# Performance work log

Hardware: AMD Instinct MI355X
Metric: run time of the kernel (lower is better)

## Reference

```python
import math
import jax, jax.numpy as jnp
import numpy as np

DEPTH, HEADS, DIM, MLP = 12, 16, 1024, 4096
J, P0, B = 17, 256, 8
N0 = J + P0
HD = DIM // HEADS
SCALE = DIM ** -0.5  # scale_with_head=False -> dim**-0.5
PRUNE_LOC = (3, 6, 9)
KEEP = 0.7


def setup_inputs() -> dict:
    key = jax.random.key(0)
    ks = jax.random.split(key, 8)
    rn = lambda k, shape, s=0.02: jax.random.normal(k, shape, dtype=jnp.float32) * s
    # rotary table (cos, sin) per position, replicated per layer: [DEPTH, N0, HD/2, 2]
    inv = 1.0 / (10000.0 ** (np.arange(0, HD, 2, dtype=np.float64) / HD))
    ang = np.arange(N0, dtype=np.float64)[:, None] * inv[None, :]
    fc = np.stack([np.cos(ang), np.sin(ang)], axis=-1)[None]
    freqs_cis = jnp.asarray(np.broadcast_to(fc, (DEPTH, N0, HD // 2, 2)), jnp.float32)
    return dict(
        x=jax.random.normal(ks[0], (B, N0, DIM), jnp.float32),
        freqs_cis=freqs_cis,
        learnable_absolute=jnp.ones((DEPTH,), jnp.float32),
        pos=rn(ks[1], (1, P0, DIM)),
        ln1_g=jnp.ones((DEPTH, DIM), jnp.float32), ln1_b=jnp.zeros((DEPTH, DIM), jnp.float32),
        w_qkv=rn(ks[2], (DEPTH, 3 * DIM, DIM)),
        w_out=rn(ks[3], (DEPTH, DIM, DIM)), b_out=jnp.zeros((DEPTH, DIM), jnp.float32),
        ln2_g=jnp.ones((DEPTH, DIM), jnp.float32), ln2_b=jnp.zeros((DEPTH, DIM), jnp.float32),
        w1=rn(ks[4], (DEPTH, MLP, DIM)), b1=jnp.zeros((DEPTH, MLP), jnp.float32),
        w2=rn(ks[5], (DEPTH, DIM, MLP)), b2=jnp.zeros((DEPTH, DIM), jnp.float32),
    )


def _ln(x, g, b, eps=1e-5):
    m = x.mean(-1, keepdims=True)
    v = ((x - m) ** 2).mean(-1, keepdims=True)
    return (x - m) * jax.lax.rsqrt(v + eps) * g + b


def _rope(t, fc):
    # t: [B,H,n,HD] viewed as complex pairs; fc: [n, HD/2, 2] = (cos, sin)
    tr = t.reshape(t.shape[:-1] + (HD // 2, 2))
    a, b_ = tr[..., 0], tr[..., 1]
    c, s = fc[..., 0], fc[..., 1]
    out = jnp.stack([a * c - b_ * s, a * s + b_ * c], axis=-1)
    return out.reshape(t.shape)


def _attn_layer(x, fc, wqkv, wout, bout, g, bb):
    Bq, n, _ = x.shape
    h = _ln(x, g, bb)  # PreNorm
    qkv = jnp.einsum('bnc,oc->bno', h, wqkv)
    q, k, v = jnp.split(qkv, 3, axis=-1)
    split = lambda t: t.reshape(Bq, n, HEADS, HD).transpose(0, 2, 1, 3)
    q, k, v = split(q), split(k), split(v)
    q, k = _rope(q, fc), _rope(k, fc)
    dots = jnp.einsum('bhid,bhjd->bhij', q * SCALE, k)
    attn = jax.nn.softmax(dots, axis=-1)
    o = jnp.einsum('bhij,bhjd->bhid', attn, v)
    o = o.transpose(0, 2, 1, 3).reshape(Bq, n, DIM)
    o = jnp.einsum('bnc,oc->bno', o, wout) + bout
    return o + x, attn  # Residual_


def _ffn_layer(x, g, bb, w1, b1, w2, b2):
    h = _ln(x, g, bb)
    h = jax.nn.gelu(jnp.einsum('bnc,hc->bnh', h, w1) + b1, approximate=False)
    return jnp.einsum('bnh,ch->bnc', h, w2) + b2 + x


def _forward(x, freqs_cis, learnable_absolute, pos, ln1_g, ln1_b, w_qkv, w_out, b_out,
             ln2_g, ln2_b, w1, b1, w2, b2):
    pos = jnp.broadcast_to(pos, (x.shape[0],) + pos.shape[1:])
    attn_res = []
    for idx in range(DEPTH):
        n = x.shape[1]
        if idx > 0:  # all_attn branch: pos rescaled cumulatively and added to patch tokens
            pos = pos * learnable_absolute[idx]
            x = x.at[:, J:].add(pos)
        fc = freqs_cis[idx, :n]
        x, attn = _attn_layer(x, fc, w_qkv[idx], w_out[idx], b_out[idx], ln1_g[idx], ln1_b[idx])
        if idx in PRUNE_LOC:  # prune=True, keep_ratio<1
            tok_attn = attn[:, :, :J, J:].sum(axis=1) / HEADS  # [B, J, P]
            human = tok_attn.sum(axis=1)                       # [B, P]
            k = math.ceil((n - J) * KEEP)
            _, top_idx = jax.lax.top_k(human, k)               # [B, k], descending-score order
            gather = lambda t: jnp.take_along_axis(t, top_idx[:, :, None], axis=1)
            x = jnp.concatenate([x[:, :J], gather(x[:, J:])], axis=1)
            pos = gather(pos)
        x = _ffn_layer(x, ln2_g[idx], ln2_b[idx], w1[idx], b1[idx], w2[idx], b2[idx])
        attn_res.append(attn)
    return x, attn_res, pos


def reference(x, freqs_cis, learnable_absolute, pos, ln1_g, ln1_b, w_qkv, w_out, b_out,
              ln2_g, ln2_b, w1, b1, w2, b2):
    x_out, attn_res, pos_out = _forward(x, freqs_cis, learnable_absolute, pos, ln1_g, ln1_b,
                                        w_qkv, w_out, b_out, ln2_g, ln2_b, w1, b1, w2, b2)
    return (x_out, *attn_res, pos_out)
```

## Files before the change

### kernel.cpp

```cpp
#include <hip/hip_runtime.h>
#include <math.h>

#define NH 16
#define HD 64
#define DM 1024
#define DMLP 4096
#define NB 8
#define JT 17
#define LN_EPS 1e-5

__global__ __launch_bounds__(256) void sentinel_kernel(float* o, float v){
  o[threadIdx.x] = v;
}

__device__ __forceinline__ double wave_sum_d(double v){
  for(int o=32;o>0;o>>=1) v += __shfl_xor(v,o);
  return v;
}
__device__ __forceinline__ double wave_max_d(double v){
  for(int o=32;o>0;o>>=1) v = fmax(v, __shfl_xor(v,o));
  return v;
}

__global__ __launch_bounds__(256) void dbcast(const float* __restrict__ src, float* __restrict__ dst){
  size_t id = (size_t)blockIdx.x*256 + threadIdx.x;
  if(id < (size_t)NB*256*DM) dst[id] = src[id % ((size_t)256*DM)];
}

__global__ __launch_bounds__(256) void dcopy(const float* __restrict__ src, float* __restrict__ dst, size_t n){
  size_t id = (size_t)blockIdx.x*256 + threadIdx.x;
  if(id < n) dst[id] = src[id];
}

__global__ __launch_bounds__(256) void dposadd(float* __restrict__ x, float* __restrict__ pos,
    const float* __restrict__ la, int l, int n, int P){
  size_t id = (size_t)blockIdx.x*256 + threadIdx.x;
  size_t tot = (size_t)NB*P*DM;
  if(id >= tot) return;
  int c = (int)(id % DM); size_t rt = id / DM;
  int p = (int)(rt % P); int b = (int)(rt / P);
  double lav = (double)la[l];
  size_t pi = ((size_t)b*P + p)*DM + c;
  double pv = (double)pos[pi] * lav;
  pos[pi] = (float)pv;
  size_t xi = ((size_t)b*n + JT + p)*DM + c;
  x[xi] = (float)((double)x[xi] + pv);
}

__global__ __launch_bounds__(256) void dln2(const float* __restrict__ x,
    const float* __restrict__ g, const float* __restrict__ bb, float* __restrict__ outp){
  __shared__ double red[8];
  size_t row = blockIdx.x;
  int tid = threadIdx.x;
  float4 v = ((const float4*)(x + row*DM))[tid];
  double s = (double)v.x + (double)v.y + (double)v.z + (double)v.w;
  s = wave_sum_d(s);
  if((tid&63)==0) red[tid>>6] = s;
  __syncthreads();
  double mean = (red[0]+red[1]+red[2]+red[3]) * (1.0/1024.0);
  double dx = (double)v.x-mean, dy = (double)v.y-mean, dz = (double)v.z-mean, dw = (double)v.w-mean;
  double sq = dx*dx+dy*dy+dz*dz+dw*dw;
  sq = wave_sum_d(sq);
  if((tid&63)==0) red[4+(tid>>6)] = sq;
  __syncthreads();
  double var = (red[4]+red[5]+red[6]+red[7]) * (1.0/1024.0);
  double inv = 1.0 / sqrt(var + LN_EPS);
  float4 gv = ((const float4*)g)[tid];
  float4 bv = ((const float4*)bb)[tid];
  float4 o;
  o.x = (float)(dx*inv*(double)gv.x + (double)bv.x);
  o.y = (float)(dy*inv*(double)gv.y + (double)bv.y);
  o.z = (float)(dz*inv*(double)gv.z + (double)bv.z);
  o.w = (float)(dw*inv*(double)gv.w + (double)bv.w);
  ((float4*)(outp + row*DM))[tid] = o;
}

__global__ __launch_bounds__(256) void ggemm(const float* __restrict__ A, const float* __restrict__ Bw,
    const float* __restrict__ bias, const float* __restrict__ res,
    float* __restrict__ C, int M, int N, int K, int act){
  __shared__ float As[32][68];
  __shared__ float Bs[32][68];
  const int tid = threadIdx.x;
  const int tx = tid & 15, ty = tid >> 4;
  const int m0 = blockIdx.y * 64, n0 = blockIdx.x * 64;
  double acc[4][4] = {};
  for(int k0 = 0; k0 < K; k0 += 32){
    #pragma unroll
    for(int r=0;r<2;r++){
      int f = tid + r*256;
      int row = f >> 3;
      int kk = (f & 7) << 2;
      int gm = m0 + row;
      float4 av = make_float4(0.f,0.f,0.f,0.f);
      if(gm < M) av = *(const float4*)(A + (size_t)gm*K + k0 + kk);
      As[kk+0][row]=av.x; As[kk+1][row]=av.y; As[kk+2][row]=av.z; As[kk+3][row]=av.w;
      float4 bv = *(const float4*)(Bw + (size_t)(n0+row)*K + k0 + kk);
      Bs[kk+0][row]=bv.x; Bs[kk+1][row]=bv.y; Bs[kk+2][row]=bv.z; Bs[kk+3][row]=bv.w;
    }
    __syncthreads();
    #pragma unroll
    for(int kk=0;kk<32;kk++){
      float4 a4 = *(const float4*)&As[kk][ty<<2];
      float4 b4 = *(const float4*)&Bs[kk][tx<<2];
      double a0=a4.x, a1=a4.y, a2=a4.z, a3=a4.w;
      double b0=b4.x, b1=b4.y, b2=b4.z, b3=b4.w;
      acc[0][0]+=a0*b0; acc[0][1]+=a0*b1; acc[0][2]+=a0*b2; acc[0][3]+=a0*b3;
      acc[1][0]+=a1*b0; acc[1][1]+=a1*b1; acc[1][2]+=a1*b2; acc[1][3]+=a1*b3;
      acc[2][0]+=a2*b0; acc[2][1]+=a2*b1; acc[2][2]+=a2*b2; acc[2][3]+=a2*b3;
      acc[3][0]+=a3*b0; acc[3][1]+=a3*b1; acc[3][2]+=a3*b2; acc[3][3]+=a3*b3;
    }
    __syncthreads();
  }
  #pragma unroll
  for(int i=0;i<4;i++){
    int gm = m0 + (ty<<2) + i;
    if(gm >= M) continue;
    int gn = n0 + (tx<<2);
    #pragma unroll
    for(int j=0;j<4;j++){
      double c = acc[i][j];
      if(bias) c += (double)bias[gn+j];
      if(act)  c = 0.5*c*(1.0 + erf(c*0.70710678118654752440));
      if(res)  c += (double)res[(size_t)gm*N + gn + j];
      C[(size_t)gm*N + gn + j] = (float)c;
    }
  }
}

__global__ __launch_bounds__(256) void drope(const float* __restrict__ qkv, const float* __restrict__ fc,
    float* __restrict__ Q, float* __restrict__ KT, float* __restrict__ V, int n){
  int id = blockIdx.x*256 + threadIdx.x;
  if(id >= NB*n*512) return;
  int pr = id & 511; int bt = id >> 9;
  int b = bt / n, t = bt % n;
  int h = pr >> 5, d2 = pr & 31;
  const float* row = qkv + (size_t)bt*3072;
  double c = (double)fc[(t*32+d2)*2], s = (double)fc[(t*32+d2)*2+1];
  double qa = (double)row[h*HD+2*d2], qb = (double)row[h*HD+2*d2+1];
  double ka = (double)row[DM + h*HD+2*d2], kb = (double)row[DM + h*HD+2*d2+1];
  size_t qoff = ((size_t)(b*NH+h)*n + t)*HD + 2*d2;
  Q[qoff]   = (float)((qa*c - qb*s)*0.03125);
  Q[qoff+1] = (float)((qa*s + qb*c)*0.03125);
  size_t koff = ((size_t)(b*NH+h)*HD + 2*d2)*n + t;
  KT[koff]     = (float)(ka*c - kb*s);
  KT[koff + n] = (float)(ka*s + kb*c);
  size_t voff = ((size_t)(b*NH+h)*n + t)*HD + 2*d2;
  V[voff]   = row[2048 + h*HD + 2*d2];
  V[voff+1] = row[2048 + h*HD + 2*d2 + 1];
}

__global__ __launch_bounds__(256) void ascore(const float* __restrict__ Q, const float* __restrict__ KT,
    float* __restrict__ attn, int n){
  int lane = threadIdx.x & 63, wv = threadIdx.x >> 6;
  int bh = blockIdx.x;
  int i = blockIdx.y*4 + wv;
  if(i >= n) return;
  float qv = Q[((size_t)bh*n + i)*HD + lane];
  const float* kb = KT + (size_t)bh*HD*n;
  double acc[5] = {0.0,0.0,0.0,0.0,0.0};
  for(int d=0; d<HD; d++){
    double qd = (double)__shfl(qv, d);
    const float* kr = kb + (size_t)d*n;
    #pragma unroll
    for(int c=0;c<5;c++){
      int j = c*64 + lane;
      acc[c] += qd * (double)(j < n ? kr[j] : 0.f);
    }
  }
  double mx = -1.0e300;
  #pragma unroll
  for(int c=0;c<5;c++) if(c*64+lane < n) mx = fmax(mx, acc[c]);
  mx = wave_max_d(mx);
  double e[5]; double sum = 0.0;
  #pragma unroll
  for(int c=0;c<5;c++){
    e[c] = (c*64+lane < n) ? exp(acc[c]-mx) : 0.0;
    sum += e[c];
  }
  sum = wave_sum_d(sum);
  double inv = 1.0/sum;
  float* arow = attn + ((size_t)bh*n + i)*n;
  #pragma unroll
  for(int c=0;c<5;c++){
    int j = c*64 + lane;
    if(j < n) arow[j] = (float)(e[c]*inv);
  }
}

__global__ __launch_bounds__(256) void apv(const float* __restrict__ attn, const float* __restrict__ V,
    float* __restrict__ O, int n){
  int lane = threadIdx.x & 63, wv = threadIdx.x >> 6;
  int bh = blockIdx.x;
  int i = blockIdx.y*4 + wv;
  if(i >= n) return;
  int b = bh >> 4, h = bh & 15;
  const float* ar = attn + ((size_t)bh*n + i)*n;
  const float* vb = V + (size_t)bh*n*HD + lane;
  double acc = 0.0;
  for(int j=0;j<n;j++)
    acc += (double)ar[j] * (double)vb[(size_t)j*HD];
  O[((size_t)(b*n + i))*DM + h*HD + lane] = (float)acc;
}

__global__ __launch_bounds__(256) void dhuman32(const float* __restrict__ attn, float* __restrict__ hum32, int n){
  int id = blockIdx.x*256 + threadIdx.x;
  int P = n - JT;
  if(id >= NB*P) return;
  int b = id / P, p = id % P;
  float s = 0.f;
  for(int i=0;i<JT;i++){
    float th = 0.f;
    for(int h=0;h<NH;h++) th += attn[(((size_t)(b*NH+h))*n + i)*n + JT + p];
    th *= 0.0625f;
    s += th;
  }
  hum32[b*256 + p] = s;
}

__global__ __launch_bounds__(256) void dselect_par(const float* __restrict__ hum, int* __restrict__ sel,
    int P, int k){
  __shared__ float v[256];
  int b = blockIdx.x, p = threadIdx.x;
  v[p] = (p < P) ? hum[b*256 + p] : -3.0e38f;
  __syncthreads();
  if(p < P){
    float mv = v[p];
    int rank = 0;
    for(int q=0;q<256;q++){
      float vq = v[q];
      rank += (vq > mv) || (vq == mv && q < p);
    }
    if(rank < k) sel[b*192 + rank] = p;
  }
}

__global__ __launch_bounds__(256) void dgather(const float* __restrict__ xin, const float* __restrict__ pin,
    const int* __restrict__ sel, float* __restrict__ xout, float* __restrict__ pout, int n_old, int k){
  int n_new = JT + k;
  size_t id = (size_t)blockIdx.x*256 + threadIdx.x;
  size_t tot = (size_t)NB*n_new*DM;
  if(id >= tot) return;
  int c = (int)(id % DM); size_t rt = id / DM;
  int t = (int)(rt % n_new); int b = (int)(rt / n_new);
  int src = (t < JT) ? t : (JT + sel[b*192 + (t-JT)]);
  xout[((size_t)b*n_new + t)*DM + c] = xin[((size_t)b*n_old + src)*DM + c];
  if(t >= JT)
    pout[((size_t)b*k + (t-JT))*DM + c] = pin[((size_t)b*(n_old-JT) + (src-JT))*DM + c];
}

extern "C" void kernel_launch(void* const* d_in, const int* in_sizes, int n_in,
                              void* d_out, int out_size, void* d_ws, size_t ws_size,
                              hipStream_t stream){
  float* out = (float*)d_out;

  const size_t NEED = 26560512ull * 4ull;
  if(ws_size < NEED){
    sentinel_kernel<<<1,256,0,stream>>>(out, 1000000.0f);
    return;
  }

  const float* x_in  = (const float*)d_in[0];
  const float* freqs = (const float*)d_in[1];
  const float* la    = (const float*)d_in[2];
  const float* pos_in= (const float*)d_in[3];
  const float* ln1g  = (const float*)d_in[4];
  const float* ln1b  = (const float*)d_in[5];
  const float* wqkv  = (const float*)d_in[6];
  const float* wout  = (const float*)d_in[7];
  const float* bout  = (const float*)d_in[8];
  const float* ln2g  = (const float*)d_in[9];
  const float* ln2b  = (const float*)d_in[10];
  const float* w1    = (const float*)d_in[11];
  const float* b1    = (const float*)d_in[12];
  const float* w2    = (const float*)d_in[13];
  const float* b2    = (const float*)d_in[14];

  float* w = (float*)d_ws;
  float* XA = w;  w += 2236416;
  float* XB = w;  w += 2236416;
  float* Hb = w;  w += 2236416;
  float* QKV= w;
  float* FF = QKV;
  float* HUM32 = QKV;
                  w += 6709248;
  float* Qb = w;  w += 2236416;
  float* Kb = w;  w += 2236416;
  float* Vb = w;  w += 2236416;
  float* Ob = w;  w += 2236416;
  float* PA = w;  w += 2097152;
  float* PB = w;  w += 2097152;
  int*   SEL = (int*)w; w += 2048;

  hipMemcpyAsync(XA, x_in, (size_t)NB*273*DM*sizeof(float), hipMemcpyDeviceToDevice, stream);
  dbcast<<<8192,256,0,stream>>>(pos_in, PA);

  float* xc = XA; float* xa = XB;
  float* pc = PA; float* pa = PB;
  int n = 273, P = 256;
  size_t aoff = 868352;

  for(int l=0;l<12;l++){
    int n_attn = n;
    if(l>0){
      size_t tot = (size_t)NB*P*DM;
      dposadd<<<(int)((tot+255)/256),256,0,stream>>>(xc, pc, la, l, n, P);
    }
    int M = NB*n;
    dln2<<<M,256,0,stream>>>(xc, ln1g + (size_t)l*DM, ln1b + (size_t)l*DM, Hb);
    ggemm<<<dim3(3072/64,(M+63)/64),256,0,stream>>>(Hb, wqkv + (size_t)l*3072*DM,
        nullptr, nullptr, QKV, M, 3072, DM, 0);
    drope<<<(NB*n*512+255)/256,256,0,stream>>>(QKV, freqs + (size_t)l*273*64, Qb, Kb, Vb, n);
    ascore<<<dim3(NB*NH,(n+3)/4),256,0,stream>>>(Qb, Kb, out + aoff, n);
    apv<<<dim3(NB*NH,(n+3)/4),256,0,stream>>>(out + aoff, Vb, Ob, n);
    ggemm<<<dim3(DM/64,(M+63)/64),256,0,stream>>>(Ob, wout + (size_t)l*DM*DM,
        bout + (size_t)l*DM, xc, xa, M, DM, DM, 0);
    { float* t=xc; xc=xa; xa=t; }
    if(l==3 || l==6 || l==9){
      int k = (P*7 + 9)/10;
      dhuman32<<<(NB*P+255)/256,256,0,stream>>>(out + aoff, HUM32, n);
      dselect_par<<<NB,256,0,stream>>>(HUM32, SEL, P, k);
      int n_new = JT + k;
      size_t tot = (size_t)NB*n_new*DM;
      dgather<<<(int)((tot+255)/256),256,0,stream>>>(xc, pc, SEL, xa, pa, n, k);
      { float* t=xc; xc=xa; xa=t; }
      { float* t=pc; pc=pa; pa=t; }
      n = n_new; P = k;
    }
    int Mf = NB*n;
    dln2<<<Mf,256,0,stream>>>(xc, ln2g + (size_t)l*DM, ln2b + (size_t)l*DM, Hb);
    ggemm<<<dim3(DMLP/64,(Mf+63)/64),256,0,stream>>>(Hb, w1 + (size_t)l*DMLP*DM,
        b1 + (size_t)l*DMLP, nullptr, FF, Mf, DMLP, DM, 1);
    ggemm<<<dim3(DM/64,(Mf+63)/64),256,0,stream>>>(FF, w2 + (size_t)l*DM*DMLP,
        b2 + (size_t)l*DM, xc, xa, Mf, DM, DMLP, 0);
    { float* t=xc; xc=xa; xa=t; }
    aoff += (size_t)128*n_attn*n_attn;
  }

  dcopy<<<(868352+255)/256,256,0,stream>>>(xc, out, 868352);
  dcopy<<<(729088+255)/256,256,0,stream>>>(pc, out + 64658688, 729088);
}
```

Measured before the change: 19.08 ms.

## Double-buffer GEMM shared tiles and use fp32 accumulation for final layers

The GEMM kernel becomes a template on accumulator type and uses double-buffered shared-memory tiles with register prefetch of the next K slice, so global loads overlap compute and one barrier per iteration is removed. GEMMs after the last pruning step (FFN from layer 9, attention from layer 10) switch from double to float accumulation, which is much cheaper on the FP64 path. Earlier layers keep double precision, likely so the top-k token selection stays exact. The trade-off is lower accuracy in the final layers and twice the shared memory per block.

After: 23.21 ms, median of 2. 21.6% more time.

```diff
diff --git a/kernel.cpp b/kernel.cpp
--- a/kernel.cpp
+++ b/kernel.cpp
@@ -75,41 +75,61 @@
   ((float4*)(outp + row*DM))[tid] = o;
 }
 
-__global__ __launch_bounds__(256) void ggemm(const float* __restrict__ A, const float* __restrict__ Bw,
+template<typename AccT>
+__global__ __launch_bounds__(256) void ggemm3(const float* __restrict__ A, const float* __restrict__ Bw,
     const float* __restrict__ bias, const float* __restrict__ res,
     float* __restrict__ C, int M, int N, int K, int act){
-  __shared__ float As[32][68];
-  __shared__ float Bs[32][68];
+  __shared__ float As[2][32][68];
+  __shared__ float Bs[2][32][68];
   const int tid = threadIdx.x;
   const int tx = tid & 15, ty = tid >> 4;
   const int m0 = blockIdx.y * 64, n0 = blockIdx.x * 64;
-  double acc[4][4] = {};
-  for(int k0 = 0; k0 < K; k0 += 32){
-    #pragma unroll
-    for(int r=0;r<2;r++){
-      int f = tid + r*256;
-      int row = f >> 3;
-      int kk = (f & 7) << 2;
-      int gm = m0 + row;
-      float4 av = make_float4(0.f,0.f,0.f,0.f);
-      if(gm < M) av = *(const float4*)(A + (size_t)gm*K + k0 + kk);
-      As[kk+0][row]=av.x; As[kk+1][row]=av.y; As[kk+2][row]=av.z; As[kk+3][row]=av.w;
-      float4 bv = *(const float4*)(Bw + (size_t)(n0+row)*K + k0 + kk);
-      Bs[kk+0][row]=bv.x; Bs[kk+1][row]=bv.y; Bs[kk+2][row]=bv.z; Bs[kk+3][row]=bv.w;
-    }
-    __syncthreads();
+  const int row0 = tid >> 3,        kk0 = (tid & 7) << 2;
+  const int row1 = (tid+256) >> 3,  kk1 = (tid & 7) << 2;
+  AccT acc[4][4] = {};
+  float4 pa0, pa1, pb0, pb1;
+  {
+    int gm0 = m0 + row0, gm1 = m0 + row1;
+    pa0 = (gm0 < M) ? *(const float4*)(A + (size_t)gm0*K + kk0) : make_float4(0.f,0.f,0.f,0.f);
+    pa1 = (gm1 < M) ? *(const float4*)(A + (size_t)gm1*K + kk1) : make_float4(0.f,0.f,0.f,0.f);
+    pb0 = *(const float4*)(Bw + (size_t)(n0+row0)*K + kk0);
+    pb1 = *(const float4*)(Bw + (size_t)(n0+row1)*K + kk1);
+  }
+  As[0][kk0+0][row0]=pa0.x; As[0][kk0+1][row0]=pa0.y; As[0][kk0+2][row0]=pa0.z; As[0][kk0+3][row0]=pa0.w;
+  As[0][kk1+0][row1]=pa1.x; As[0][kk1+1][row1]=pa1.y; As[0][kk1+2][row1]=pa1.z; As[0][kk1+3][row1]=pa1.w;
+  Bs[0][kk0+0][row0]=pb0.x; Bs[0][kk0+1][row0]=pb0.y; Bs[0][kk0+2][row0]=pb0.z; Bs[0][kk0+3][row0]=pb0.w;
+  Bs[0][kk1+0][row1]=pb1.x; Bs[0][kk1+1][row1]=pb1.y; Bs[0][kk1+2][row1]=pb1.z; Bs[0][kk1+3][row1]=pb1.w;
+  __syncthreads();
+  const int nT = K >> 5;
+  for(int t=0; t<nT; ++t){
+    const int cb = t & 1;
+    if(t+1 < nT){
+      const int k0 = (t+1) << 5;
+      int gm0 = m0 + row0, gm1 = m0 + row1;
+      pa0 = (gm0 < M) ? *(const float4*)(A + (size_t)gm0*K + k0 + kk0) : make_float4(0.f,0.f,0.f,0.f);
+      pa1 = (gm1 < M) ? *(const float4*)(A + (size_t)gm1*K + k0 + kk1) : make_float4(0.f,0.f,0.f,0.f);
+      pb0 = *(const float4*)(Bw + (size_t)(n0+row0)*K + k0 + kk0);
+      pb1 = *(const float4*)(Bw + (size_t)(n0+row1)*K + k0 + kk1);
+    }
     #pragma unroll
     for(int kk=0;kk<32;kk++){
-      float4 a4 = *(const float4*)&As[kk][ty<<2];
-      float4 b4 = *(const float4*)&Bs[kk][tx<<2];
-      double a0=a4.x, a1=a4.y, a2=a4.z, a3=a4.w;
-      double b0=b4.x, b1=b4.y, b2=b4.z, b3=b4.w;
+      float4 a4 = *(const float4*)&As[cb][kk][ty<<2];
+      float4 b4 = *(const float4*)&Bs[cb][kk][tx<<2];
+      AccT a0=(AccT)a4.x, a1=(AccT)a4.y, a2=(AccT)a4.z, a3=(AccT)a4.w;
+      AccT b0=(AccT)b4.x, b1=(AccT)b4.y, b2=(AccT)b4.z, b3=(AccT)b4.w;
       acc[0][0]+=a0*b0; acc[0][1]+=a0*b1; acc[0][2]+=a0*b2; acc[0][3]+=a0*b3;
       acc[1][0]+=a1*b0; acc[1][1]+=a1*b1; acc[1][2]+=a1*b2; acc[1][3]+=a1*b3;
       acc[2][0]+=a2*b0; acc[2][1]+=a2*b1; acc[2][2]+=a2*b2; acc[2][3]+=a2*b3;
       acc[3][0]+=a3*b0; acc[3][1]+=a3*b1; acc[3][2]+=a3*b2; acc[3][3]+=a3*b3;
     }
-    __syncthreads();
+    if(t+1 < nT){
+      const int nb = cb ^ 1;
+      As[nb][kk0+0][row0]=pa0.x; As[nb][kk0+1][row0]=pa0.y; As[nb][kk0+2][row0]=pa0.z; As[nb][kk0+3][row0]=pa0.w;
+      As[nb][kk1+0][row1]=pa1.x; As[nb][kk1+1][row1]=pa1.y; As[nb][kk1+2][row1]=pa1.z; As[nb][kk1+3][row1]=pa1.w;
+      Bs[nb][kk0+0][row0]=pb0.x; Bs[nb][kk0+1][row0]=pb0.y; Bs[nb][kk0+2][row0]=pb0.z; Bs[nb][kk0+3][row0]=pb0.w;
+      Bs[nb][kk1+0][row1]=pb1.x; Bs[nb][kk1+1][row1]=pb1.y; Bs[nb][kk1+2][row1]=pb1.z; Bs[nb][kk1+3][row1]=pb1.w;
+      __syncthreads();
+    }
   }
   #pragma unroll
   for(int i=0;i<4;i++){
@@ -118,11 +138,19 @@
     int gn = n0 + (tx<<2);
     #pragma unroll
     for(int j=0;j<4;j++){
-      double c = acc[i][j];
-      if(bias) c += (double)bias[gn+j];
-      if(act)  c = 0.5*c*(1.0 + erf(c*0.70710678118654752440));
-      if(res)  c += (double)res[(size_t)gm*N + gn + j];
-      C[(size_t)gm*N + gn + j] = (float)c;
+      if(sizeof(AccT) == 8){
+        double c = (double)acc[i][j];
+        if(bias) c += (double)bias[gn+j];
+        if(act)  c = 0.5*c*(1.0 + erf(c*0.70710678118654752440));
+        if(res)  c += (double)res[(size_t)gm*N + gn + j];
+        C[(size_t)gm*N + gn + j] = (float)c;
+      } else {
+        float c = (float)acc[i][j];
+        if(bias) c += bias[gn+j];
+        if(act)  c = 0.5f*c*(1.0f + erff(c*0.70710678f));
+        if(res)  c += res[(size_t)gm*N + gn + j];
+        C[(size_t)gm*N + gn + j] = c;
+      }
     }
   }
 }
@@ -248,6 +276,15 @@
     pout[((size_t)b*k + (t-JT))*DM + c] = pin[((size_t)b*(n_old-JT) + (src-JT))*DM + c];
 }
 
+static inline void launch_gemm(const float* A, const float* Bw, const float* bias,
+    const float* res, float* C, int M, int N, int K, int act, bool fp32, hipStream_t stream){
+  dim3 grid(N/64, (M+63)/64);
+  if(fp32)
+    ggemm3<float ><<<grid,256,0,stream>>>(A, Bw, bias, res, C, M, N, K, act);
+  else
+    ggemm3<double><<<grid,256,0,stream>>>(A, Bw, bias, res, C, M, N, K, act);
+}
+
 extern "C" void kernel_launch(void* const* d_in, const int* in_sizes, int n_in,
                               void* d_out, int out_size, void* d_ws, size_t ws_size,
                               hipStream_t stream){
@@ -301,19 +338,18 @@
 
   for(int l=0;l<12;l++){
     int n_attn = n;
+    bool free_layer = (l >= 10);
     if(l>0){
       size_t tot = (size_t)NB*P*DM;
       dposadd<<<(int)((tot+255)/256),256,0,stream>>>(xc, pc, la, l, n, P);
     }
     int M = NB*n;
     dln2<<<M,256,0,stream>>>(xc, ln1g + (size_t)l*DM, ln1b + (size_t)l*DM, Hb);
-    ggemm<<<dim3(3072/64,(M+63)/64),256,0,stream>>>(Hb, wqkv + (size_t)l*3072*DM,
-        nullptr, nullptr, QKV, M, 3072, DM, 0);
+    launch_gemm(Hb, wqkv + (size_t)l*3072*DM, nullptr, nullptr, QKV, M, 3072, DM, 0, free_layer, stream);
     drope<<<(NB*n*512+255)/256,256,0,stream>>>(QKV, freqs + (size_t)l*273*64, Qb, Kb, Vb, n);
     ascore<<<dim3(NB*NH,(n+3)/4),256,0,stream>>>(Qb, Kb, out + aoff, n);
     apv<<<dim3(NB*NH,(n+3)/4),256,0,stream>>>(out + aoff, Vb, Ob, n);
-    ggemm<<<dim3(DM/64,(M+63)/64),256,0,stream>>>(Ob, wout + (size_t)l*DM*DM,
-        bout + (size_t)l*DM, xc, xa, M, DM, DM, 0);
+    launch_gemm(Ob, wout + (size_t)l*DM*DM, bout + (size_t)l*DM, xc, xa, M, DM, DM, 0, free_layer, stream);
     { float* t=xc; xc=xa; xa=t; }
     if(l==3 || l==6 || l==9){
       int k = (P*7 + 9)/10;
@@ -326,12 +362,11 @@
       { float* t=pc; pc=pa; pa=t; }
       n = n_new; P = k;
     }
+    bool free_ffn = (l >= 9);
     int Mf = NB*n;
     dln2<<<Mf,256,0,stream>>>(xc, ln2g + (size_t)l*DM, ln2b + (size_t)l*DM, Hb);
-    ggemm<<<dim3(DMLP/64,(Mf+63)/64),256,0,stream>>>(Hb, w1 + (size_t)l*DMLP*DM,
-        b1 + (size_t)l*DMLP, nullptr, FF, Mf, DMLP, DM, 1);
-    ggemm<<<dim3(DM/64,(Mf+63)/64),256,0,stream>>>(FF, w2 + (size_t)l*DM*DMLP,
-        b2 + (size_t)l*DM, xc, xa, Mf, DM, DMLP, 0);
+    launch_gemm(Hb, w1 + (size_t)l*DMLP*DM, b1 + (size_t)l*DMLP, nullptr, FF, Mf, DMLP, DM, 1, free_ffn, stream);
+    launch_gemm(FF, w2 + (size_t)l*DM*DMLP, b2 + (size_t)l*DM, xc, xa, Mf, DM, DMLP, 0, free_ffn, stream);
     { float* t=xc; xc=xa; xa=t; }
     aoff += (size_t)128*n_attn*n_attn;
   }
```
